# Kernel optimization log

Measured on AMD Instinct MI355X. Metric: run time of the kernel, lower is better.

The kernel has to match this reference:

```python
import jax, jax.numpy as jnp
import numpy as np

POLY_WEIGHT = 1.0  # init kwarg poly_weight
B, A, K = 32, 262144, 131072


def setup_inputs() -> dict:
    key = jax.random.key(0)
    k1, k2, k3, k4 = jax.random.split(key, 4)
    inp = jax.random.normal(k1, (B, 2 * K), dtype=jnp.float32)
    xy = jax.random.normal(k2, (B, A, 2), dtype=jnp.float32)
    idx = jax.random.randint(k3, (B, A), 0, K).astype(jnp.float32)
    state = (jax.random.uniform(k4, (B, A)) < 0.5).astype(jnp.float32)
    target = jnp.concatenate([xy, idx[..., None], state[..., None]], axis=-1)
    return {"input": inp, "target": target}


def _smooth_l1(d):
    ad = jnp.abs(d)
    return jnp.where(ad < 1.0, 0.5 * d * d, ad - 0.5)


def reference(input, target):
    Bk = input.shape[0]
    Kk = input.shape[1] // 2
    regression = input.reshape(Bk, 2, Kk)          # (B, 2, K)
    reg_target = target[:, :, 0:2]                  # (B, A, 2)
    idx = target[:, :, 2].astype(jnp.int32)         # (B, A) indices into K
    mask = (target[:, :, 3] == 1.0)                 # (B, A) positive anchors

    reg_bk2 = jnp.transpose(regression, (0, 2, 1))  # (B, K, 2)
    idx_c = jnp.clip(idx, 0, Kk - 1)
    gathered = jnp.take_along_axis(reg_bk2, idx_c[:, :, None], axis=1)  # (B, A, 2)

    per = _smooth_l1(gathered - reg_target)         # (B, A, 2)
    maskf = mask.astype(per.dtype)
    poly_loss = jnp.sum(per * maskf[:, :, None])
    normalizer = jnp.maximum(jnp.float32(1.0), jnp.sum(maskf))
    return poly_loss / normalizer * POLY_WEIGHT
```

## Files before the change

kernel.cpp:

```cpp
#include <hip/hip_runtime.h>

#define B_BATCH   32
#define A_ELEMS   262144
#define A_SHIFT   18
#define K_ELEMS   131072
#define NPOS      ((long long)B_BATCH * A_ELEMS)

typedef float v4f __attribute__((ext_vector_type(4)));

__global__ void zero_ws_kernel(float* ws) {
    ws[0] = 0.0f;
    ws[1] = 0.0f;
}

__global__ __launch_bounds__(256) void regloss_batched_kernel(
    const float* __restrict__ input,
    const v4f*  __restrict__ target,
    float* __restrict__ ws)
{
    const int tid = threadIdx.x;
    const int xcd = blockIdx.x & 7;
    const int j   = blockIdx.x >> 3;

    float loss = 0.0f;
    float cnt  = 0.0f;

    #pragma unroll
    for (int g = 0; g < 4; ++g) {
        const int batch = xcd + 8 * g;
        const float* __restrict__ inb = input + (size_t)batch * (2 * K_ELEMS);
        const size_t pos = (size_t)batch * A_ELEMS + (size_t)j * 1024
                         + (size_t)tid * 4;

        v4f t[4];
        #pragma unroll
        for (int u = 0; u < 4; ++u)
            t[u] = __builtin_nontemporal_load(&target[pos + u]);

        float g0[4], g1[4], m[4];
        #pragma unroll
        for (int u = 0; u < 4; ++u) {
            int idx = (int)t[u].z;
            idx = min(max(idx, 0), K_ELEMS - 1);
            g0[u] = inb[idx];
            g1[u] = inb[K_ELEMS + idx];
            m[u]  = (t[u].w == 1.0f) ? 1.0f : 0.0f;
        }

        #pragma unroll
        for (int u = 0; u < 4; ++u) {
            float dx = g0[u] - t[u].x;
            float dy = g1[u] - t[u].y;
            float adx = fabsf(dx), ady = fabsf(dy);
            float lx = (adx < 1.0f) ? 0.5f * dx * dx : adx - 0.5f;
            float ly = (ady < 1.0f) ? 0.5f * dy * dy : ady - 0.5f;
            loss += m[u] * (lx + ly);
            cnt  += m[u];
        }
    }

    #pragma unroll
    for (int off = 32; off > 0; off >>= 1) {
        loss += __shfl_down(loss, off, 64);
        cnt  += __shfl_down(cnt,  off, 64);
    }
    __shared__ float sl[4], sc[4];
    const int wave = tid >> 6, lane = tid & 63;
    if (lane == 0) { sl[wave] = loss; sc[wave] = cnt; }
    __syncthreads();
    if (tid == 0) {
        atomicAdd(&ws[0], sl[0] + sl[1] + sl[2] + sl[3]);
        atomicAdd(&ws[1], sc[0] + sc[1] + sc[2] + sc[3]);
    }
}

__global__ __launch_bounds__(256) void regloss_generic_kernel(
    const float* __restrict__ input,
    const v4f* __restrict__ target,
    float* __restrict__ ws,
    long long N, int K, int ashift)
{
    long long tid    = (long long)blockIdx.x * blockDim.x + threadIdx.x;
    long long stride = (long long)gridDim.x * blockDim.x;
    float loss = 0.0f, cnt = 0.0f;
    for (long long i = tid; i < N; i += stride) {
        v4f t = target[i];
        if (t.w == 1.0f) {
            int b   = (int)(i >> ashift);
            int idx = min(max((int)t.z, 0), K - 1);
            const float* inb = input + (long long)b * (2LL * K);
            float dx = inb[idx] - t.x;
            float dy = inb[K + idx] - t.y;
            float adx = fabsf(dx), ady = fabsf(dy);
            loss += (adx < 1.0f) ? 0.5f * dx * dx : adx - 0.5f;
            loss += (ady < 1.0f) ? 0.5f * dy * dy : ady - 0.5f;
            cnt  += 1.0f;
        }
    }
    #pragma unroll
    for (int off = 32; off > 0; off >>= 1) {
        loss += __shfl_down(loss, off, 64);
        cnt  += __shfl_down(cnt,  off, 64);
    }
    __shared__ float sl[4], sc[4];
    int wave = threadIdx.x >> 6, lane = threadIdx.x & 63;
    if (lane == 0) { sl[wave] = loss; sc[wave] = cnt; }
    __syncthreads();
    if (threadIdx.x == 0) {
        atomicAdd(&ws[0], sl[0] + sl[1] + sl[2] + sl[3]);
        atomicAdd(&ws[1], sc[0] + sc[1] + sc[2] + sc[3]);
    }
}

__global__ void finalize_kernel(const float* __restrict__ ws,
                                float* __restrict__ out) {
    const float POLY_WEIGHT = 1.0f;
    out[0] = ws[0] / fmaxf(1.0f, ws[1]) * POLY_WEIGHT;
}

extern "C" void kernel_launch(void* const* d_in, const int* in_sizes, int n_in,
                              void* d_out, int out_size, void* d_ws, size_t ws_size,
                              hipStream_t stream) {
    const float* input  = (const float*)d_in[0];
    const v4f*   target = (const v4f*)d_in[1];
    float* out = (float*)d_out;
    float* ws  = (float*)d_ws;

    long long N = (long long)in_sizes[1] / 4;

    zero_ws_kernel<<<1, 1, 0, stream>>>(ws);

    if (N == NPOS && in_sizes[0] == 2 * K_ELEMS * B_BATCH) {
        regloss_batched_kernel<<<2048, 256, 0, stream>>>(input, target, ws);
    } else {
        regloss_generic_kernel<<<2048, 256, 0, stream>>>(input, target, ws,
                                                         N, K_ELEMS, A_SHIFT);
    }

    finalize_kernel<<<1, 1, 0, stream>>>(ws, out);
}
```

Before: 295.4 us.

## Interleave regression planes into workspace and prefetch next target batch

```diff
diff --git a/kernel.cpp b/kernel.cpp
--- a/kernel.cpp
+++ b/kernel.cpp
@@ -5,17 +5,38 @@
 #define A_SHIFT   18
 #define K_ELEMS   131072
 #define NPOS      ((long long)B_BATCH * A_ELEMS)
+#define WS_T_OFF  64
+#define WS_NEED   ((size_t)(WS_T_OFF + 2 * B_BATCH * K_ELEMS) * 4)
 
 typedef float v4f __attribute__((ext_vector_type(4)));
+typedef float v2f __attribute__((ext_vector_type(2)));
 
 __global__ void zero_ws_kernel(float* ws) {
     ws[0] = 0.0f;
     ws[1] = 0.0f;
 }
 
+__global__ __launch_bounds__(256) void transpose_kernel(
+    const float* __restrict__ input,
+    v2f* __restrict__ wsT)
+{
+    const long long base = (long long)blockIdx.x * 2048 + threadIdx.x;
+    #pragma unroll
+    for (int s = 0; s < 8; ++s) {
+        long long flat = base + (long long)s * 256;
+        int b = (int)(flat >> 17);
+        int k = (int)(flat & (K_ELEMS - 1));
+        const float* inb = input + (size_t)b * (2 * K_ELEMS);
+        v2f v;
+        v.x = inb[k];
+        v.y = inb[K_ELEMS + k];
+        wsT[flat] = v;
+    }
+}
+
 __global__ __launch_bounds__(256) void regloss_batched_kernel(
-    const float* __restrict__ input,
-    const v4f*  __restrict__ target,
+    const v2f* __restrict__ wsT,
+    const v4f* __restrict__ target,
     float* __restrict__ ws)
 {
     const int tid = threadIdx.x;
@@ -25,37 +46,55 @@
     float loss = 0.0f;
     float cnt  = 0.0f;
 
+    v4f tcur[4];
+    {
+        const int batch = xcd;
+        const size_t pos = (size_t)batch * A_ELEMS + (size_t)j * 1024 + (size_t)tid * 4;
+        #pragma unroll
+        for (int u = 0; u < 4; ++u)
+            tcur[u] = __builtin_nontemporal_load(&target[pos + u]);
+    }
+
     #pragma unroll
     for (int g = 0; g < 4; ++g) {
         const int batch = xcd + 8 * g;
-        const float* __restrict__ inb = input + (size_t)batch * (2 * K_ELEMS);
-        const size_t pos = (size_t)batch * A_ELEMS + (size_t)j * 1024
-                         + (size_t)tid * 4;
+        const v2f* __restrict__ wb = wsT + (size_t)batch * K_ELEMS;
 
-        v4f t[4];
-        #pragma unroll
-        for (int u = 0; u < 4; ++u)
-            t[u] = __builtin_nontemporal_load(&target[pos + u]);
-
-        float g0[4], g1[4], m[4];
+        v2f gv[4];
+        float m[4];
         #pragma unroll
         for (int u = 0; u < 4; ++u) {
-            int idx = (int)t[u].z;
+            int idx = (int)tcur[u].z;
             idx = min(max(idx, 0), K_ELEMS - 1);
-            g0[u] = inb[idx];
-            g1[u] = inb[K_ELEMS + idx];
-            m[u]  = (t[u].w == 1.0f) ? 1.0f : 0.0f;
+            m[u] = (tcur[u].w == 1.0f) ? 1.0f : 0.0f;
+            v2f g2; g2.x = 0.0f; g2.y = 0.0f;
+            if (m[u] != 0.0f) g2 = wb[idx];
+            gv[u] = g2;
+        }
+
+        v4f tnext[4];
+        if (g < 3) {
+            const int nb = xcd + 8 * (g + 1);
+            const size_t pos = (size_t)nb * A_ELEMS + (size_t)j * 1024 + (size_t)tid * 4;
+            #pragma unroll
+            for (int u = 0; u < 4; ++u)
+                tnext[u] = __builtin_nontemporal_load(&target[pos + u]);
         }
 
         #pragma unroll
         for (int u = 0; u < 4; ++u) {
-            float dx = g0[u] - t[u].x;
-            float dy = g1[u] - t[u].y;
+            float dx = gv[u].x - tcur[u].x;
+            float dy = gv[u].y - tcur[u].y;
             float adx = fabsf(dx), ady = fabsf(dy);
             float lx = (adx < 1.0f) ? 0.5f * dx * dx : adx - 0.5f;
             float ly = (ady < 1.0f) ? 0.5f * dy * dy : ady - 0.5f;
             loss += m[u] * (lx + ly);
             cnt  += m[u];
+        }
+
+        if (g < 3) {
+            #pragma unroll
+            for (int u = 0; u < 4; ++u) tcur[u] = tnext[u];
         }
     }
 
@@ -130,8 +169,11 @@
 
     zero_ws_kernel<<<1, 1, 0, stream>>>(ws);
 
-    if (N == NPOS && in_sizes[0] == 2 * K_ELEMS * B_BATCH) {
-        regloss_batched_kernel<<<2048, 256, 0, stream>>>(input, target, ws);
+    const bool shapes_ok = (N == NPOS) && (in_sizes[0] == 2 * K_ELEMS * B_BATCH);
+    if (shapes_ok && ws_size >= WS_NEED) {
+        v2f* wsT = (v2f*)(ws + WS_T_OFF);
+        transpose_kernel<<<2048, 256, 0, stream>>>(input, wsT);
+        regloss_batched_kernel<<<2048, 256, 0, stream>>>(wsT, target, ws);
     } else {
         regloss_generic_kernel<<<2048, 256, 0, stream>>>(input, target, ws,
                                                          N, K_ELEMS, A_SHIFT);
```

Result: faster. 260.1 us (-11.9%).
